# Kernel optimization log

Hardware: AMD Instinct MI355X
Metric: run time of the kernel (lower is better)

Reference implementation:

```python
import jax, jax.numpy as jnp
import numpy as np

N, L, K, Dc, Db, Dd, C = 4096, 32, 8, 64, 64, 16, 8
B, M = 32, 1000  # M_samples hardcoded to 1000 in the original forward
LOG2PI = float(np.log(2.0 * np.pi))


def setup_inputs() -> dict:
    key = jax.random.key(0)
    ks = jax.random.split(key, 16)
    X_c = jax.random.normal(ks[0], (B, Dc), dtype=jnp.float32)
    X_b = (jax.random.uniform(ks[1], (B, Db)) < 0.5).astype(jnp.float32)
    X_d = jax.random.randint(ks[2], (B, Dd), 0, C, dtype=jnp.int32)
    # variational / posterior parameters (as in __init__)
    q_z_mean = jax.random.uniform(ks[3], (N, L), dtype=jnp.float32)
    q_log_var = jax.random.uniform(ks[4], (N, L), dtype=jnp.float32)
    g = jax.random.uniform(ks[5], (N, K), dtype=jnp.float32) + 1e-3
    q_s_param = g / jnp.sum(g, axis=-1, keepdims=True)  # Dirichlet-like rows
    posterior_mean = jnp.zeros((N, L), dtype=jnp.float32)
    posterior_var = jnp.ones((N, L), dtype=jnp.float32)
    posterior_mu = jnp.ones((N, K), dtype=jnp.float32) / K
    # heterogeneous FA likelihood params (per component k)
    s = 1.0 / np.sqrt(L)
    W_g = jax.random.normal(ks[6], (K, Dc, L), dtype=jnp.float32) * s
    b_g = jax.random.normal(ks[7], (K, Dc), dtype=jnp.float32) * 0.1
    logvar_g = jax.random.normal(ks[8], (K, Dc), dtype=jnp.float32) * 0.1
    W_b = jax.random.normal(ks[9], (K, Db, L), dtype=jnp.float32) * s
    b_b = jax.random.normal(ks[10], (K, Db), dtype=jnp.float32) * 0.1
    W_d = jax.random.normal(ks[11], (K, Dd, C, L), dtype=jnp.float32) * s
    b_d = jax.random.normal(ks[12], (K, Dd, C), dtype=jnp.float32) * 0.1
    eps = jax.random.normal(ks[13], (B, M, L), dtype=jnp.float32)  # rsample noise
    return dict(index=0, X_c=X_c, X_b=X_b, X_d=X_d,
                q_z_mean=q_z_mean, q_log_var=q_log_var, q_s_param=q_s_param,
                posterior_mean=posterior_mean, posterior_var=posterior_var,
                posterior_mu=posterior_mu,
                W_g=W_g, b_g=b_g, logvar_g=logvar_g,
                W_b=W_b, b_b=b_b, W_d=W_d, b_d=b_d, eps=eps)


def _log_liks(z, X_c, X_b, X_d, W_g, b_g, logvar_g, W_b, b_b, W_d, b_d):
    # z: [B,M,L] -> each term [B,K,M] (log_pdf summed over feature dims)
    mean = jnp.einsum('kdl,bml->bkmd', W_g, z) + b_g[None, :, None, :]
    var = jnp.exp(logvar_g)[None, :, None, :]
    t1 = -0.5 * jnp.sum(LOG2PI + logvar_g[None, :, None, :]
                        + (X_c[:, None, None, :] - mean) ** 2 / var, axis=-1)
    logits_b = jnp.einsum('kdl,bml->bkmd', W_b, z) + b_b[None, :, None, :]
    t2 = jnp.sum(X_b[:, None, None, :] * logits_b - jax.nn.softplus(logits_b), axis=-1)
    logits_d = jnp.einsum('kdcl,bml->bkmdc', W_d, z) + b_d[None, :, None, :, :]
    logp = jax.nn.log_softmax(logits_d, axis=-1)  # [B,K,M,Dd,C]
    idx = jnp.broadcast_to(X_d[:, None, None, :, None].astype(jnp.int32),
                           logp.shape[:-1] + (1,))
    t3 = jnp.sum(jnp.take_along_axis(logp, idx, axis=-1)[..., 0], axis=-1)
    return t1, t2, t3


def reference(index, X_c, X_b, X_d, q_z_mean, q_log_var, q_s_param,
              posterior_mean, posterior_var, posterior_mu,
              W_g, b_g, logvar_g, W_b, b_b, W_d, b_d, eps):
    start = B * index
    end = start + B
    qm = q_z_mean[start:end]        # [B,L]
    qlv = q_log_var[start:end]      # [B,L]
    qs = q_s_param[start:end]       # [B,K]
    mp = posterior_mean[start:end]
    vp = posterior_var[start:end]
    pmu = posterior_mu[start:end]
    # reparameterized MC samples z ~ q_z
    z = qm[:, None, :] + jnp.exp(0.5 * qlv)[:, None, :] * eps  # [B,M,L]
    t1, t2, t3 = _log_liks(z, X_c, X_b, X_d, W_g, b_g, logvar_g, W_b, b_b, W_d, b_d)
    # LL_i = sum_k q_s[i,k] * sum_m (t1+t2+t3)  (sum, no /M, as in original)
    LL = jnp.sum(qs * jnp.sum(t1 + t2 + t3, axis=-1))
    # KL(q_z || p_z), both diagonal MVNs
    vq = jnp.exp(qlv)
    klz = 0.5 * jnp.sum(jnp.log(vp) - qlv + (vq + (qm - mp) ** 2) / vp - 1.0, axis=-1)
    # KL(q_s || p_s), Categorical normalizes probs
    qn = qs / jnp.sum(qs, axis=-1, keepdims=True)
    pn = pmu / jnp.sum(pmu, axis=-1, keepdims=True)
    kls = jnp.sum(qn * (jnp.log(qn) - jnp.log(pn)), axis=-1)
    elbo = LL - jnp.sum(klz) - jnp.sum(kls)
    KL_z = klz[-1]   # original returns last iteration's KL
    KL_s = kls[-1]
    term_1 = jnp.sum(t1, axis=(0, 1))  # [M]
    term_2 = jnp.sum(t2, axis=(0, 1))
    term_3 = jnp.sum(t3, axis=(0, 1))
    rik = jnp.zeros((N, K), dtype=jnp.float32).at[start:end].set(
        jax.nn.softmax(qs, axis=-1))
    rik = jax.lax.stop_gradient(rik)
    return (-elbo, LL, KL_z, KL_s, rik, term_1, term_2, term_3)
```

## Files before the change

### kernel.cpp

```cpp
#include <hip/hip_runtime.h>
#include <math.h>

#define N_ 4096
#define L_ 32
#define K_ 8
#define Dc_ 64
#define Db_ 64
#define Dd_ 16
#define C_ 8
#define B_ 32
#define M_ 1000
#define LOG2PI_ 1.8378770664093453f

#define OUT_RIK 4
#define OUT_T1 (4 + N_ * K_)

#define WS_PART 0
#define WS_LLP  98304
#define WS_WP   99328
#define WS_BIAS (WS_WP + 32768)
#define WS_IV   (WS_BIAS + 2048)
#define WS_C1   (WS_IV + 512)

typedef __attribute__((ext_vector_type(8))) short short8v;
typedef __attribute__((ext_vector_type(4))) float f32x4;

__device__ inline unsigned short f2bf(float f) {
    unsigned u = __builtin_bit_cast(unsigned, f);
    unsigned r = u + 0x7FFFu + ((u >> 16) & 1u);
    return (unsigned short)(r >> 16);
}

#define PW  65536
#define PB  (PW + 2048)
#define PIV (PB + 512)
#define PC1 (PIV + 9)

__global__ __launch_bounds__(256) void mm_prep(
    const float* __restrict__ Wg, const float* __restrict__ bg, const float* __restrict__ lvg,
    const float* __restrict__ Wb, const float* __restrict__ bb,
    const float* __restrict__ Wd, const float* __restrict__ bd,
    float* __restrict__ ws)
{
    const int t = blockIdx.x * 256 + threadIdx.x;
    unsigned short* wpw = (unsigned short*)(ws + WS_WP);

    if (t < PW) {
        int j = t & 7, lane = (t >> 3) & 63, ft = (t >> 9) & 15, k = t >> 13;
        int f = ft * 16 + (lane & 15);
        int l = (lane >> 4) * 8 + j;
        float w;
        if (f < 64)       w = Wg[((size_t)k * 64 + f) * L_ + l];
        else if (f < 128) w = Wb[((size_t)k * 64 + (f - 64)) * L_ + l];
        else { int d = (f - 128) >> 3, c = f & 7; w = Wd[(((size_t)k * 16 + d) * 8 + c) * L_ + l]; }
        wpw[t] = f2bf(w);
    } else if (t < PB) {
        int i = t - PW; int k = i >> 8, f = i & 255;
        float v;
        if (f < 64)       v = bg[k * 64 + f];
        else if (f < 128) v = bb[k * 64 + f - 64];
        else { int d = (f - 128) >> 3, c = f & 7; v = bd[(k * 16 + d) * 8 + c]; }
        ws[WS_BIAS + i] = v;
    } else if (t < PIV) {
        int i = t - PB;
        ws[WS_IV + i] = __expf(-lvg[i]);
    } else if (t < PC1) {
        int k = t - PIV;
        if (k < 8) {
            float s = 0.f;
            for (int d = 0; d < 64; ++d) s += LOG2PI_ + lvg[k * 64 + d];
            ws[WS_C1 + k] = s;
        } else {
            float s = 0.f;
            for (int i = 0; i < 512; ++i) s += LOG2PI_ + lvg[i];
            ws[WS_C1 + 8] = s;
        }
    }
}

__global__ __launch_bounds__(512) void mm_main(
    const int* __restrict__ pidx,
    const float* __restrict__ Xc, const float* __restrict__ Xb, const int* __restrict__ Xd,
    const float* __restrict__ qm_all, const float* __restrict__ qlv_all,
    const float* __restrict__ qs_all, const float* __restrict__ eps,
    float* __restrict__ ws)
{
    const int tid = threadIdx.x, w = tid >> 6, lane = tid & 63;
    const int mt = blockIdx.x, b = blockIdx.y;
    const int l15 = lane & 15, lg = lane >> 4;
    const int fr = 4 * lg;
    const int start = B_ * pidx[0];
    const unsigned short* wp = (const unsigned short*)(ws + WS_WP);

    __shared__ __align__(16) unsigned int zu[512];
    __shared__ __align__(16) float scin[2048];
    __shared__ __align__(16) float siv[512];
    __shared__ float sqk[8];
    __shared__ float sred[8][2][2][16];
    __shared__ float llred[8];

    if (tid < 256) {
        int m_loc = tid >> 3, l0 = (tid & 7) * 4;
        int m_glob = mt * 32 + m_loc;
        float4 e = make_float4(0.f, 0.f, 0.f, 0.f);
        if (m_glob < M_) e = *(const float4*)(eps + ((size_t)b * M_ + m_glob) * L_ + l0);
        float4 qm4 = *(const float4*)(qm_all + (size_t)(start + b) * L_ + l0);
        float4 ql4 = *(const float4*)(qlv_all + (size_t)(start + b) * L_ + l0);
        float z0 = qm4.x + __expf(0.5f * ql4.x) * e.x;
        float z1 = qm4.y + __expf(0.5f * ql4.y) * e.y;
        float z2 = qm4.z + __expf(0.5f * ql4.z) * e.z;
        float z3 = qm4.w + __expf(0.5f * ql4.w) * e.w;
        unsigned u0 = (unsigned)f2bf(z0) | ((unsigned)f2bf(z1) << 16);
        unsigned u1 = (unsigned)f2bf(z2) | ((unsigned)f2bf(z3) << 16);
        int widx = (m_loc >> 4) * 256 + ((l0 >> 3) * 16 + (m_loc & 15)) * 4 + ((l0 & 7) >> 1);
        zu[widx] = u0; zu[widx + 1] = u1;
    }
    {
        int f = (tid & 63) * 4;
        float4 bv = *(const float4*)(ws + WS_BIAS + tid * 4);
        if (f < 64) {
            float4 xc = *(const float4*)(Xc + b * 64 + f);
            bv.x -= xc.x; bv.y -= xc.y; bv.z -= xc.z; bv.w -= xc.w;
        }
        ((float4*)scin)[tid] = bv;
    }
    if (tid < 128) ((float4*)siv)[tid] = *(const float4*)(ws + WS_IV + tid * 4);
    if (tid < 8)   sqk[tid] = qs_all[(size_t)(start + b) * K_ + tid];
    __syncthreads();

    const short8v zb0 = *(const short8v*)((const unsigned short*)zu + lane * 8);
    const short8v zb1 = *(const short8v*)((const unsigned short*)zu + 512 + lane * 8);

    const float4 xf = *(const float4*)(Xb + b * 64 + (w & 3) * 16 + fr);
    const int d3 = 2 * w + (lg >> 1);
    const int xd = Xd[b * 16 + d3];
    const int cc0 = 4 * (lg & 1);
    float4 is3;
    is3.x = (cc0 + 0 == xd) ? 1.f : 0.f;  is3.y = (cc0 + 1 == xd) ? 1.f : 0.f;
    is3.z = (cc0 + 2 == xd) ? 1.f : 0.f;  is3.w = (cc0 + 3 == xd) ? 1.f : 0.f;

    float ta0 = 0.f, ta1 = 0.f, tb0 = 0.f, tb1 = 0.f, ll0 = 0.f, ll1 = 0.f;

    #pragma unroll 2
    for (int k = 0; k < K_; ++k) {
        const short8v wfA = *(const short8v*)(wp + ((size_t)(k * 16 + w))     * 512 + lane * 8);
        const short8v wfB = *(const short8v*)(wp + ((size_t)(k * 16 + 8 + w)) * 512 + lane * 8);
        const float4 cA = *(const float4*)(scin + k * 256 + w * 16 + fr);
        const float4 cB = *(const float4*)(scin + k * 256 + (8 + w) * 16 + fr);
        const float qkv = sqk[k];

        const f32x4 ciA = {cA.x, cA.y, cA.z, cA.w};
        const f32x4 ciB = {cB.x, cB.y, cB.z, cB.w};
        f32x4 d00 = __builtin_amdgcn_mfma_f32_16x16x32_bf16(wfA, zb0, ciA, 0, 0, 0);
        f32x4 d01 = __builtin_amdgcn_mfma_f32_16x16x32_bf16(wfA, zb1, ciA, 0, 0, 0);
        f32x4 d10 = __builtin_amdgcn_mfma_f32_16x16x32_bf16(wfB, zb0, ciB, 0, 0, 0);
        f32x4 d11 = __builtin_amdgcn_mfma_f32_16x16x32_bf16(wfB, zb1, ciB, 0, 0, 0);

        if (w < 4) {
            const float4 iv4 = *(const float4*)(siv + k * 64 + w * 16 + fr);
            float s0 = 0.f, s1 = 0.f;
            s0 = fmaf(d00[0] * d00[0], iv4.x, s0); s1 = fmaf(d01[0] * d01[0], iv4.x, s1);
            s0 = fmaf(d00[1] * d00[1], iv4.y, s0); s1 = fmaf(d01[1] * d01[1], iv4.y, s1);
            s0 = fmaf(d00[2] * d00[2], iv4.z, s0); s1 = fmaf(d01[2] * d01[2], iv4.z, s1);
            s0 = fmaf(d00[3] * d00[3], iv4.w, s0); s1 = fmaf(d01[3] * d01[3], iv4.w, s1);
            ta0 += s0; ta1 += s1;
            const float qm5 = -0.5f * qkv;
            ll0 = fmaf(qm5, s0, ll0); ll1 = fmaf(qm5, s1, ll1);
        } else {
            float s0 = 0.f, s1 = 0.f, lgt, sp;
            lgt = d00[0]; sp = fmaxf(lgt, 0.f) + __logf(1.f + __expf(-fabsf(lgt))); s0 += xf.x * lgt - sp;
            lgt = d00[1]; sp = fmaxf(lgt, 0.f) + __logf(1.f + __expf(-fabsf(lgt))); s0 += xf.y * lgt - sp;
            lgt = d00[2]; sp = fmaxf(lgt, 0.f) + __logf(1.f + __expf(-fabsf(lgt))); s0 += xf.z * lgt - sp;
            lgt = d00[3]; sp = fmaxf(lgt, 0.f) + __logf(1.f + __expf(-fabsf(lgt))); s0 += xf.w * lgt - sp;
            lgt = d01[0]; sp = fmaxf(lgt, 0.f) + __logf(1.f + __expf(-fabsf(lgt))); s1 += xf.x * lgt - sp;
            lgt = d01[1]; sp = fmaxf(lgt, 0.f) + __logf(1.f + __expf(-fabsf(lgt))); s1 += xf.y * lgt - sp;
            lgt = d01[2]; sp = fmaxf(lgt, 0.f) + __logf(1.f + __expf(-fabsf(lgt))); s1 += xf.z * lgt - sp;
            lgt = d01[3]; sp = fmaxf(lgt, 0.f) + __logf(1.f + __expf(-fabsf(lgt))); s1 += xf.w * lgt - sp;
            ta0 += s0; ta1 += s1;
            ll0 = fmaf(qkv, s0, ll0); ll1 = fmaf(qkv, s1, ll1);
        }

        {
            float e4 = __expf(d10[0]) + __expf(d10[1]) + __expf(d10[2]) + __expf(d10[3]);
            float se = e4 + __shfl_xor(e4, 16, 64);
            float u  = is3.x * d10[0] + is3.y * d10[1] + is3.z * d10[2] + is3.w * d10[3];
            float tm = u - 0.5f * __logf(se);
            tb0 += tm; ll0 = fmaf(qkv, tm, ll0);
        }
        {
            float e4 = __expf(d11[0]) + __expf(d11[1]) + __expf(d11[2]) + __expf(d11[3]);
            float se = e4 + __shfl_xor(e4, 16, 64);
            float u  = is3.x * d11[0] + is3.y * d11[1] + is3.z * d11[2] + is3.w * d11[3];
            float tm = u - 0.5f * __logf(se);
            tb1 += tm; ll1 = fmaf(qkv, tm, ll1);
        }
    }

    const bool ok0 = (mt * 32 + l15)      < M_;
    const bool ok1 = (mt * 32 + 16 + l15) < M_;
    if (!ok0) { ta0 = 0.f; tb0 = 0.f; ll0 = 0.f; }
    if (!ok1) { ta1 = 0.f; tb1 = 0.f; ll1 = 0.f; }

    float tar0 = ta0 + __shfl_xor(ta0, 16, 64); tar0 += __shfl_xor(tar0, 32, 64);
    float tar1 = ta1 + __shfl_xor(ta1, 16, 64); tar1 += __shfl_xor(tar1, 32, 64);
    float tbr0 = tb0 + __shfl_xor(tb0, 16, 64); tbr0 += __shfl_xor(tbr0, 32, 64);
    float tbr1 = tb1 + __shfl_xor(tb1, 16, 64); tbr1 += __shfl_xor(tbr1, 32, 64);
    float llv = ll0 + ll1;
    #pragma unroll
    for (int ofs = 1; ofs < 64; ofs <<= 1) llv += __shfl_xor(llv, ofs, 64);

    if (lane < 16) {
        sred[w][0][0][l15] = tar0; sred[w][1][0][l15] = tar1;
        sred[w][0][1][l15] = tbr0; sred[w][1][1][l15] = tbr1;
    }
    if (lane == 0) llred[w] = llv;
    __syncthreads();

    if (tid < 96) {
        int i = tid >> 5, tile = (tid >> 4) & 1, cx = tid & 15;
        int rt = mt * 2 + tile, m = rt * 16 + cx;
        float vout;
        if (i == 0) {
            float s = sred[0][tile][0][cx] + sred[1][tile][0][cx]
                    + sred[2][tile][0][cx] + sred[3][tile][0][cx];
            vout = (m < M_) ? (-0.5f * (ws[WS_C1 + 8] + s)) : 0.f;
        } else if (i == 1) {
            vout = sred[4][tile][0][cx] + sred[5][tile][0][cx]
                 + sred[6][tile][0][cx] + sred[7][tile][0][cx];
        } else {
            vout = 0.f;
            #pragma unroll
            for (int ww = 0; ww < 8; ++ww) vout += sred[ww][tile][1][cx];
        }
        ws[WS_PART + ((size_t)b * 64 + rt) * 48 + i * 16 + cx] = vout;
    }
    if (tid == 96) {
        float s = 0.f;
        #pragma unroll
        for (int ww = 0; ww < 8; ++ww) s += llred[ww];
        float cterm = 0.f;
        #pragma unroll
        for (int k = 0; k < 8; ++k) cterm = fmaf(sqk[k], ws[WS_C1 + k], cterm);
        int nv = M_ - mt * 32; nv = (nv > 32) ? 32 : (nv < 0 ? 0 : nv);
        ws[WS_LLP + b * 32 + mt] = s - 0.5f * cterm * (float)nv;
    }
}

__global__ __launch_bounds__(256) void mm_final(
    const int* __restrict__ pidx,
    const float* __restrict__ qm_all, const float* __restrict__ qlv_all,
    const float* __restrict__ qs_all,
    const float* __restrict__ pm_all, const float* __restrict__ pv_all,
    const float* __restrict__ pmu_all,
    const float* __restrict__ ws, float* __restrict__ out)
{
    const int tid = threadIdx.x;
    if (blockIdx.x == 0) {
        __shared__ float wred[4];
        __shared__ float skl[B_], sks[B_];
        const int start = B_ * pidx[0];
        float v = ws[WS_LLP + tid] + ws[WS_LLP + 256 + tid]
                + ws[WS_LLP + 512 + tid] + ws[WS_LLP + 768 + tid];
        #pragma unroll
        for (int ofs = 1; ofs < 64; ofs <<= 1) v += __shfl_xor(v, ofs, 64);
        if ((tid & 63) == 0) wred[tid >> 6] = v;

        if (tid < B_) {
            int r = start + tid;
            float kl = 0.f;
            for (int l = 0; l < L_; ++l) {
                float qmv = qm_all[(size_t)r * L_ + l];
                float qlv = qlv_all[(size_t)r * L_ + l];
                float mp  = pm_all[(size_t)r * L_ + l];
                float vp  = pv_all[(size_t)r * L_ + l];
                float d   = qmv - mp;
                kl += __logf(vp) - qlv + (__expf(qlv) + d * d) / vp - 1.f;
            }
            skl[tid] = 0.5f * kl;

            float qsum = 0.f, psum = 0.f;
            #pragma unroll
            for (int j = 0; j < K_; ++j) {
                qsum += qs_all[(size_t)r * K_ + j];
                psum += pmu_all[(size_t)r * K_ + j];
            }
            float ks = 0.f;
            #pragma unroll
            for (int j = 0; j < K_; ++j) {
                float qn = qs_all[(size_t)r * K_ + j] / qsum;
                float pn = pmu_all[(size_t)r * K_ + j] / psum;
                ks += qn * (__logf(qn) - __logf(pn));
            }
            sks[tid] = ks;
        }
        __syncthreads();
        if (tid == 0) {
            float LL = wred[0] + wred[1] + wred[2] + wred[3];
            float sklz = 0.f, skls = 0.f;
            for (int i = 0; i < B_; ++i) { sklz += skl[i]; skls += sks[i]; }
            float elbo = LL - sklz - skls;
            out[0] = -elbo;
            out[1] = LL;
            out[2] = skl[B_ - 1];
            out[3] = sks[B_ - 1];
        }
    } else if (blockIdx.x <= 12) {
        int g = (blockIdx.x - 1) * 256 + tid;
        if (g < 3 * M_) {
            int i = g / M_, m = g % M_;
            int rt = m >> 4, cx = m & 15;
            float s = 0.f;
            #pragma unroll 8
            for (int b2 = 0; b2 < 32; ++b2)
                s += ws[WS_PART + ((size_t)b2 * 64 + rt) * 48 + i * 16 + cx];
            out[OUT_T1 + i * M_ + m] = s;
        }
    } else {
        int i = (blockIdx.x - 13) * 256 + tid;
        int r = i >> 3, c = i & 7;
        int start = B_ * pidx[0];
        float v = 0.f;
        if (r >= start && r < start + B_) {
            const float* row = qs_all + (size_t)r * K_;
            float mx = row[0];
            #pragma unroll
            for (int jj = 1; jj < K_; ++jj) mx = fmaxf(mx, row[jj]);
            float se = 0.f;
            #pragma unroll
            for (int jj = 0; jj < K_; ++jj) se += __expf(row[jj] - mx);
            v = __expf(row[c] - mx) / se;
        }
        out[OUT_RIK + i] = v;
    }
}

extern "C" void kernel_launch(void* const* d_in, const int* in_sizes, int n_in,
                              void* d_out, int out_size, void* d_ws, size_t ws_size,
                              hipStream_t stream)
{
    (void)in_sizes; (void)n_in; (void)out_size; (void)ws_size;
    const int*   pidx = (const int*)d_in[0];
    const float* Xc   = (const float*)d_in[1];
    const float* Xb   = (const float*)d_in[2];
    const int*   Xd   = (const int*)d_in[3];
    const float* qm   = (const float*)d_in[4];
    const float* qlv  = (const float*)d_in[5];
    const float* qs   = (const float*)d_in[6];
    const float* pm   = (const float*)d_in[7];
    const float* pv   = (const float*)d_in[8];
    const float* pmu  = (const float*)d_in[9];
    const float* Wg   = (const float*)d_in[10];
    const float* bg   = (const float*)d_in[11];
    const float* lvg  = (const float*)d_in[12];
    const float* Wb   = (const float*)d_in[13];
    const float* bb   = (const float*)d_in[14];
    const float* Wd   = (const float*)d_in[15];
    const float* bd   = (const float*)d_in[16];
    const float* eps  = (const float*)d_in[17];
    float* out = (float*)d_out;
    float* ws  = (float*)d_ws;

    mm_prep<<<(PC1 + 255) / 256, 256, 0, stream>>>(Wg, bg, lvg, Wb, bb, Wd, bd, ws);

    dim3 grid(32, 32);
    mm_main<<<grid, 512, 0, stream>>>(pidx, Xc, Xb, Xd, qm, qlv, qs, eps, ws);

    mm_final<<<141, 256, 0, stream>>>(pidx, qm, qlv, qs, pm, pv, pmu, ws, out);
}
```

Baseline: 42.25 us.

## Fuse prep, main and final kernels into one with last-block atomic reduction

Removes the separate weight-packing prep kernel and the final reduction kernel. The main kernel now reads fp32 weights directly and converts them to bf16 in registers, computes bias and inverse-variance tables inline, and writes the rik softmax rows. The final reductions run in the last block to finish, detected with atomic counters that a memset zeroes before launch. This saves two kernel launches and the intermediate workspace round trip. In exchange every block repeats the weight loads and conversions, and the reduction tail is serialized on the last-arriving blocks.

```diff
diff --git a/kernel.cpp b/kernel.cpp
--- a/kernel.cpp
+++ b/kernel.cpp
@@ -1,4 +1,5 @@
 #include <hip/hip_runtime.h>
+#include <hip/hip_bf16.h>
 #include <math.h>
 
 #define N_ 4096
@@ -17,10 +18,7 @@
 
 #define WS_PART 0
 #define WS_LLP  98304
-#define WS_WP   99328
-#define WS_BIAS (WS_WP + 32768)
-#define WS_IV   (WS_BIAS + 2048)
-#define WS_C1   (WS_IV + 512)
+#define WS_CNT  99328
 
 typedef __attribute__((ext_vector_type(8))) short short8v;
 typedef __attribute__((ext_vector_type(4))) float f32x4;
@@ -31,66 +29,39 @@
     return (unsigned short)(r >> 16);
 }
 
-#define PW  65536
-#define PB  (PW + 2048)
-#define PIV (PB + 512)
-#define PC1 (PIV + 9)
-
-__global__ __launch_bounds__(256) void mm_prep(
+__device__ inline unsigned short bf16u(float x) {
+    __hip_bfloat16 h = __float2bfloat16(x);
+    return __builtin_bit_cast(unsigned short, h);
+}
+
+__device__ inline short8v cvt8(float4 a, float4 b) {
+    short8v r;
+    r[0] = (short)bf16u(a.x); r[1] = (short)bf16u(a.y);
+    r[2] = (short)bf16u(a.z); r[3] = (short)bf16u(a.w);
+    r[4] = (short)bf16u(b.x); r[5] = (short)bf16u(b.y);
+    r[6] = (short)bf16u(b.z); r[7] = (short)bf16u(b.w);
+    return r;
+}
+
+__global__ __launch_bounds__(512) void mm_fused(
+    const int* __restrict__ pidx,
+    const float* __restrict__ Xc, const float* __restrict__ Xb, const int* __restrict__ Xd,
+    const float* __restrict__ qm_all, const float* __restrict__ qlv_all,
+    const float* __restrict__ qs_all,
+    const float* __restrict__ pm_all, const float* __restrict__ pv_all,
+    const float* __restrict__ pmu_all,
     const float* __restrict__ Wg, const float* __restrict__ bg, const float* __restrict__ lvg,
     const float* __restrict__ Wb, const float* __restrict__ bb,
     const float* __restrict__ Wd, const float* __restrict__ bd,
-    float* __restrict__ ws)
-{
-    const int t = blockIdx.x * 256 + threadIdx.x;
-    unsigned short* wpw = (unsigned short*)(ws + WS_WP);
-
-    if (t < PW) {
-        int j = t & 7, lane = (t >> 3) & 63, ft = (t >> 9) & 15, k = t >> 13;
-        int f = ft * 16 + (lane & 15);
-        int l = (lane >> 4) * 8 + j;
-        float w;
-        if (f < 64)       w = Wg[((size_t)k * 64 + f) * L_ + l];
-        else if (f < 128) w = Wb[((size_t)k * 64 + (f - 64)) * L_ + l];
-        else { int d = (f - 128) >> 3, c = f & 7; w = Wd[(((size_t)k * 16 + d) * 8 + c) * L_ + l]; }
-        wpw[t] = f2bf(w);
-    } else if (t < PB) {
-        int i = t - PW; int k = i >> 8, f = i & 255;
-        float v;
-        if (f < 64)       v = bg[k * 64 + f];
-        else if (f < 128) v = bb[k * 64 + f - 64];
-        else { int d = (f - 128) >> 3, c = f & 7; v = bd[(k * 16 + d) * 8 + c]; }
-        ws[WS_BIAS + i] = v;
-    } else if (t < PIV) {
-        int i = t - PB;
-        ws[WS_IV + i] = __expf(-lvg[i]);
-    } else if (t < PC1) {
-        int k = t - PIV;
-        if (k < 8) {
-            float s = 0.f;
-            for (int d = 0; d < 64; ++d) s += LOG2PI_ + lvg[k * 64 + d];
-            ws[WS_C1 + k] = s;
-        } else {
-            float s = 0.f;
-            for (int i = 0; i < 512; ++i) s += LOG2PI_ + lvg[i];
-            ws[WS_C1 + 8] = s;
-        }
-    }
-}
-
-__global__ __launch_bounds__(512) void mm_main(
-    const int* __restrict__ pidx,
-    const float* __restrict__ Xc, const float* __restrict__ Xb, const int* __restrict__ Xd,
-    const float* __restrict__ qm_all, const float* __restrict__ qlv_all,
-    const float* __restrict__ qs_all, const float* __restrict__ eps,
-    float* __restrict__ ws)
+    const float* __restrict__ eps,
+    float* __restrict__ out, float* __restrict__ ws)
 {
     const int tid = threadIdx.x, w = tid >> 6, lane = tid & 63;
     const int mt = blockIdx.x, b = blockIdx.y;
     const int l15 = lane & 15, lg = lane >> 4;
     const int fr = 4 * lg;
     const int start = B_ * pidx[0];
-    const unsigned short* wp = (const unsigned short*)(ws + WS_WP);
+    unsigned* cnt = (unsigned*)(ws + WS_CNT);
 
     __shared__ __align__(16) unsigned int zu[512];
     __shared__ __align__(16) float scin[2048];
@@ -98,6 +69,9 @@
     __shared__ float sqk[8];
     __shared__ float sred[8][2][2][16];
     __shared__ float llred[8];
+    __shared__ int sflag;
+    __shared__ float sfin[8], sll[8], sc1k[8], sllc[4];
+    __shared__ float skl2[B_], sks2[B_];
 
     if (tid < 256) {
         int m_loc = tid >> 3, l0 = (tid & 7) * 4;
@@ -116,16 +90,27 @@
         zu[widx] = u0; zu[widx + 1] = u1;
     }
     {
-        int f = (tid & 63) * 4;
-        float4 bv = *(const float4*)(ws + WS_BIAS + tid * 4);
+        int k = tid >> 6, f = (tid & 63) * 4;
+        float4 bv;
         if (f < 64) {
+            bv = *(const float4*)(bg + k * 64 + f);
             float4 xc = *(const float4*)(Xc + b * 64 + f);
             bv.x -= xc.x; bv.y -= xc.y; bv.z -= xc.z; bv.w -= xc.w;
+        } else if (f < 128) {
+            bv = *(const float4*)(bb + k * 64 + (f - 64));
+        } else {
+            bv = *(const float4*)(bd + k * 128 + (f - 128));
         }
         ((float4*)scin)[tid] = bv;
     }
-    if (tid < 128) ((float4*)siv)[tid] = *(const float4*)(ws + WS_IV + tid * 4);
-    if (tid < 8)   sqk[tid] = qs_all[(size_t)(start + b) * K_ + tid];
+    if (tid < 128) {
+        float4 lv4 = *(const float4*)(lvg + tid * 4);
+        float4 r;
+        r.x = __expf(-lv4.x); r.y = __expf(-lv4.y);
+        r.z = __expf(-lv4.z); r.w = __expf(-lv4.w);
+        ((float4*)siv)[tid] = r;
+    }
+    if (tid < 8) sqk[tid] = qs_all[(size_t)(start + b) * K_ + tid];
     __syncthreads();
 
     const short8v zb0 = *(const short8v*)((const unsigned short*)zu + lane * 8);
@@ -139,12 +124,20 @@
     is3.x = (cc0 + 0 == xd) ? 1.f : 0.f;  is3.y = (cc0 + 1 == xd) ? 1.f : 0.f;
     is3.z = (cc0 + 2 == xd) ? 1.f : 0.f;  is3.w = (cc0 + 3 == xd) ? 1.f : 0.f;
 
+    const float* baseA = (w < 4) ? Wg : Wb;
+    const size_t offA = (size_t)((w & 3) * 16 + l15) * 32 + lg * 8;
+    const size_t offB = (size_t)(w * 16 + l15) * 32 + lg * 8;
+
     float ta0 = 0.f, ta1 = 0.f, tb0 = 0.f, tb1 = 0.f, ll0 = 0.f, ll1 = 0.f;
 
     #pragma unroll 2
     for (int k = 0; k < K_; ++k) {
-        const short8v wfA = *(const short8v*)(wp + ((size_t)(k * 16 + w))     * 512 + lane * 8);
-        const short8v wfB = *(const short8v*)(wp + ((size_t)(k * 16 + 8 + w)) * 512 + lane * 8);
+        float4 ra0 = *(const float4*)(baseA + k * 2048 + offA);
+        float4 ra1 = *(const float4*)(baseA + k * 2048 + offA + 4);
+        float4 rb0 = *(const float4*)(Wd + k * 4096 + offB);
+        float4 rb1 = *(const float4*)(Wd + k * 4096 + offB + 4);
+        const short8v wfA = cvt8(ra0, ra1);
+        const short8v wfB = cvt8(rb0, rb1);
         const float4 cA = *(const float4*)(scin + k * 256 + w * 16 + fr);
         const float4 cB = *(const float4*)(scin + k * 256 + (8 + w) * 16 + fr);
         const float qkv = sqk[k];
@@ -218,12 +211,11 @@
 
     if (tid < 96) {
         int i = tid >> 5, tile = (tid >> 4) & 1, cx = tid & 15;
-        int rt = mt * 2 + tile, m = rt * 16 + cx;
+        int rt = mt * 2 + tile;
         float vout;
         if (i == 0) {
-            float s = sred[0][tile][0][cx] + sred[1][tile][0][cx]
-                    + sred[2][tile][0][cx] + sred[3][tile][0][cx];
-            vout = (m < M_) ? (-0.5f * (ws[WS_C1 + 8] + s)) : 0.f;
+            vout = sred[0][tile][0][cx] + sred[1][tile][0][cx]
+                 + sred[2][tile][0][cx] + sred[3][tile][0][cx];
         } else if (i == 1) {
             vout = sred[4][tile][0][cx] + sred[5][tile][0][cx]
                  + sred[6][tile][0][cx] + sred[7][tile][0][cx];
@@ -238,33 +230,78 @@
         float s = 0.f;
         #pragma unroll
         for (int ww = 0; ww < 8; ++ww) s += llred[ww];
-        float cterm = 0.f;
-        #pragma unroll
-        for (int k = 0; k < 8; ++k) cterm = fmaf(sqk[k], ws[WS_C1 + k], cterm);
-        int nv = M_ - mt * 32; nv = (nv > 32) ? 32 : (nv < 0 ? 0 : nv);
-        ws[WS_LLP + b * 32 + mt] = s - 0.5f * cterm * (float)nv;
-    }
-}
-
-__global__ __launch_bounds__(256) void mm_final(
-    const int* __restrict__ pidx,
-    const float* __restrict__ qm_all, const float* __restrict__ qlv_all,
-    const float* __restrict__ qs_all,
-    const float* __restrict__ pm_all, const float* __restrict__ pv_all,
-    const float* __restrict__ pmu_all,
-    const float* __restrict__ ws, float* __restrict__ out)
-{
-    const int tid = threadIdx.x;
-    if (blockIdx.x == 0) {
-        __shared__ float wred[4];
-        __shared__ float skl[B_], sks[B_];
-        const int start = B_ * pidx[0];
-        float v = ws[WS_LLP + tid] + ws[WS_LLP + 256 + tid]
-                + ws[WS_LLP + 512 + tid] + ws[WS_LLP + 768 + tid];
+        ws[WS_LLP + b * 32 + mt] = s;
+    }
+
+    if (tid < 32) {
+        int i = (b * 32 + mt) * 32 + tid;
+        int r = i >> 3, c = i & 7;
+        float v = 0.f;
+        if (r >= start && r < start + B_) {
+            const float* row = qs_all + (size_t)r * K_;
+            float mx = row[0];
+            #pragma unroll
+            for (int jj = 1; jj < K_; ++jj) mx = fmaxf(mx, row[jj]);
+            float se = 0.f;
+            #pragma unroll
+            for (int jj = 0; jj < K_; ++jj) se += __expf(row[jj] - mx);
+            v = __expf(row[c] - mx) / se;
+        }
+        out[OUT_RIK + i] = v;
+    }
+
+    __syncthreads();
+    if (tid == 0) {
+        __threadfence();
+        unsigned o1 = atomicAdd(cnt + mt, 1u);
+        unsigned o2 = atomicAdd(cnt + 32, 1u);
+        sflag = ((o1 == 31u) ? 1 : 0) | ((o2 == 1023u) ? 2 : 0);
+    }
+    __syncthreads();
+    const int flg = sflag;
+
+    if (flg & 1) {
+        __threadfence();
+        float c1v = LOG2PI_ + lvg[tid];
+        #pragma unroll
+        for (int ofs = 1; ofs < 64; ofs <<= 1) c1v += __shfl_xor(c1v, ofs, 64);
+        if (lane == 0) sfin[w] = c1v;
+        __syncthreads();
+        float C1sum = 0.f;
+        #pragma unroll
+        for (int ww = 0; ww < 8; ++ww) C1sum += sfin[ww];
+        if (tid < 96) {
+            int i = tid >> 5, cx = tid & 31;
+            int m = mt * 32 + cx;
+            if (m < M_) {
+                int rt = mt * 2 + (cx >> 4), cxx = cx & 15;
+                float s = 0.f;
+                #pragma unroll 8
+                for (int b2 = 0; b2 < 32; ++b2)
+                    s += ws[WS_PART + ((size_t)b2 * 64 + rt) * 48 + i * 16 + cxx];
+                float vout = (i == 0) ? (-0.5f * (32.f * C1sum + s)) : s;
+                out[OUT_T1 + i * M_ + m] = vout;
+            }
+        }
+    }
+
+    if (flg & 2) {
+        __threadfence();
+        float v = ws[WS_LLP + tid] + ws[WS_LLP + 512 + tid];
         #pragma unroll
         for (int ofs = 1; ofs < 64; ofs <<= 1) v += __shfl_xor(v, ofs, 64);
-        if ((tid & 63) == 0) wred[tid >> 6] = v;
-
+        if (lane == 0) sll[w] = v;
+        float c1v = LOG2PI_ + lvg[tid];
+        #pragma unroll
+        for (int ofs = 1; ofs < 64; ofs <<= 1) c1v += __shfl_xor(c1v, ofs, 64);
+        if (lane == 0) sc1k[w] = c1v;
+        __syncthreads();
+        if (tid < 256) {
+            float lc = qs_all[(size_t)(start + (tid >> 3)) * K_ + (tid & 7)] * sc1k[tid & 7];
+            #pragma unroll
+            for (int ofs = 1; ofs < 64; ofs <<= 1) lc += __shfl_xor(lc, ofs, 64);
+            if (lane == 0) sllc[w] = lc;
+        }
         if (tid < B_) {
             int r = start + tid;
             float kl = 0.f;
@@ -276,8 +313,7 @@
                 float d   = qmv - mp;
                 kl += __logf(vp) - qlv + (__expf(qlv) + d * d) / vp - 1.f;
             }
-            skl[tid] = 0.5f * kl;
-
+            skl2[tid] = 0.5f * kl;
             float qsum = 0.f, psum = 0.f;
             #pragma unroll
             for (int j = 0; j < K_; ++j) {
@@ -291,46 +327,25 @@
                 float pn = pmu_all[(size_t)r * K_ + j] / psum;
                 ks += qn * (__logf(qn) - __logf(pn));
             }
-            sks[tid] = ks;
+            sks2[tid] = ks;
         }
         __syncthreads();
         if (tid == 0) {
-            float LL = wred[0] + wred[1] + wred[2] + wred[3];
+            float LL = 0.f;
+            #pragma unroll
+            for (int ww = 0; ww < 8; ++ww) LL += sll[ww];
+            float lcs = 0.f;
+            #pragma unroll
+            for (int ww = 0; ww < 4; ++ww) lcs += sllc[ww];
+            LL -= 0.5f * (float)M_ * lcs;
             float sklz = 0.f, skls = 0.f;
-            for (int i = 0; i < B_; ++i) { sklz += skl[i]; skls += sks[i]; }
+            for (int i = 0; i < B_; ++i) { sklz += skl2[i]; skls += sks2[i]; }
             float elbo = LL - sklz - skls;
             out[0] = -elbo;
             out[1] = LL;
-            out[2] = skl[B_ - 1];
-            out[3] = sks[B_ - 1];
-        }
-    } else if (blockIdx.x <= 12) {
-        int g = (blockIdx.x - 1) * 256 + tid;
-        if (g < 3 * M_) {
-            int i = g / M_, m = g % M_;
-            int rt = m >> 4, cx = m & 15;
-            float s = 0.f;
-            #pragma unroll 8
-            for (int b2 = 0; b2 < 32; ++b2)
-                s += ws[WS_PART + ((size_t)b2 * 64 + rt) * 48 + i * 16 + cx];
-            out[OUT_T1 + i * M_ + m] = s;
-        }
-    } else {
-        int i = (blockIdx.x - 13) * 256 + tid;
-        int r = i >> 3, c = i & 7;
-        int start = B_ * pidx[0];
-        float v = 0.f;
-        if (r >= start && r < start + B_) {
-            const float* row = qs_all + (size_t)r * K_;
-            float mx = row[0];
-            #pragma unroll
-            for (int jj = 1; jj < K_; ++jj) mx = fmaxf(mx, row[jj]);
-            float se = 0.f;
-            #pragma unroll
-            for (int jj = 0; jj < K_; ++jj) se += __expf(row[jj] - mx);
-            v = __expf(row[c] - mx) / se;
-        }
-        out[OUT_RIK + i] = v;
+            out[2] = skl2[B_ - 1];
+            out[3] = sks2[B_ - 1];
+        }
     }
 }
 
@@ -360,10 +375,10 @@
     float* out = (float*)d_out;
     float* ws  = (float*)d_ws;
 
-    mm_prep<<<(PC1 + 255) / 256, 256, 0, stream>>>(Wg, bg, lvg, Wb, bb, Wd, bd, ws);
+    hipMemsetAsync((char*)d_ws + (size_t)WS_CNT * 4, 0, 33 * 4, stream);
 
     dim3 grid(32, 32);
-    mm_main<<<grid, 512, 0, stream>>>(pidx, Xc, Xb, Xd, qm, qlv, qs, eps, ws);
-
-    mm_final<<<141, 256, 0, stream>>>(pidx, qm, qlv, qs, pm, pv, pmu, ws, out);
-}
+    mm_fused<<<grid, 512, 0, stream>>>(pidx, Xc, Xb, Xd, qm, qlv, qs,
+                                       pm, pv, pmu, Wg, bg, lvg, Wb, bb, Wd, bd,
+                                       eps, out, ws);
+}
```

New measurement: 79.23 us. 1.88x slower.

## Process 64 samples per block to reuse weight fragments across four MFMA tiles

Applied to the files above, without the earlier changes.

Each mm_main block now covers 64 Monte Carlo samples instead of 32. Every loaded weight fragment and bias feeds four MFMAs instead of two, and the grid shrinks to 16x32 blocks, with launch_bounds set to request two blocks per CU. The Gaussian constant offset moves from mm_main into mm_final's reduction, scaled by the batch size. The intent is to halve weight loads and block setup, at the cost of more registers per thread and fewer blocks (512) to spread over the CUs.

```diff
diff --git a/kernel.cpp b/kernel.cpp
--- a/kernel.cpp
+++ b/kernel.cpp
@@ -78,7 +78,7 @@
     }
 }
 
-__global__ __launch_bounds__(512) void mm_main(
+__global__ __launch_bounds__(512, 2) void mm_main(
     const int* __restrict__ pidx,
     const float* __restrict__ Xc, const float* __restrict__ Xb, const int* __restrict__ Xd,
     const float* __restrict__ qm_all, const float* __restrict__ qlv_all,
@@ -92,16 +92,16 @@
     const int start = B_ * pidx[0];
     const unsigned short* wp = (const unsigned short*)(ws + WS_WP);
 
-    __shared__ __align__(16) unsigned int zu[512];
+    __shared__ __align__(16) unsigned int zu[1024];
     __shared__ __align__(16) float scin[2048];
     __shared__ __align__(16) float siv[512];
     __shared__ float sqk[8];
-    __shared__ float sred[8][2][2][16];
+    __shared__ float sred[8][4][2][16];
     __shared__ float llred[8];
 
-    if (tid < 256) {
+    {
         int m_loc = tid >> 3, l0 = (tid & 7) * 4;
-        int m_glob = mt * 32 + m_loc;
+        int m_glob = mt * 64 + m_loc;
         float4 e = make_float4(0.f, 0.f, 0.f, 0.f);
         if (m_glob < M_) e = *(const float4*)(eps + ((size_t)b * M_ + m_glob) * L_ + l0);
         float4 qm4 = *(const float4*)(qm_all + (size_t)(start + b) * L_ + l0);
@@ -128,8 +128,11 @@
     if (tid < 8)   sqk[tid] = qs_all[(size_t)(start + b) * K_ + tid];
     __syncthreads();
 
-    const short8v zb0 = *(const short8v*)((const unsigned short*)zu + lane * 8);
-    const short8v zb1 = *(const short8v*)((const unsigned short*)zu + 512 + lane * 8);
+    const unsigned short* zp = (const unsigned short*)zu;
+    const short8v zbA = *(const short8v*)(zp + lane * 8);
+    const short8v zbB = *(const short8v*)(zp + 512 + lane * 8);
+    const short8v zbC = *(const short8v*)(zp + 1024 + lane * 8);
+    const short8v zbD = *(const short8v*)(zp + 1536 + lane * 8);
 
     const float4 xf = *(const float4*)(Xb + b * 64 + (w & 3) * 16 + fr);
     const int d3 = 2 * w + (lg >> 1);
@@ -139,7 +142,32 @@
     is3.x = (cc0 + 0 == xd) ? 1.f : 0.f;  is3.y = (cc0 + 1 == xd) ? 1.f : 0.f;
     is3.z = (cc0 + 2 == xd) ? 1.f : 0.f;  is3.w = (cc0 + 3 == xd) ? 1.f : 0.f;
 
-    float ta0 = 0.f, ta1 = 0.f, tb0 = 0.f, tb1 = 0.f, ll0 = 0.f, ll1 = 0.f;
+    float taA = 0.f, taB = 0.f, taC = 0.f, taD = 0.f;
+    float tbA = 0.f, tbB = 0.f, tbC = 0.f, tbD = 0.f;
+    float llA = 0.f, llB = 0.f, llC = 0.f, llD = 0.f;
+
+#define GAUSS_EPI(dd, ta_, ll_) { \
+    float s_ = 0.f; \
+    s_ = fmaf(dd[0] * dd[0], iv4.x, s_); \
+    s_ = fmaf(dd[1] * dd[1], iv4.y, s_); \
+    s_ = fmaf(dd[2] * dd[2], iv4.z, s_); \
+    s_ = fmaf(dd[3] * dd[3], iv4.w, s_); \
+    ta_ += s_; ll_ = fmaf(qm5, s_, ll_); }
+
+#define BERN_EPI(dd, ta_, ll_) { \
+    float s_ = 0.f, lgt_, sp_; \
+    lgt_ = dd[0]; sp_ = fmaxf(lgt_, 0.f) + __logf(1.f + __expf(-fabsf(lgt_))); s_ += xf.x * lgt_ - sp_; \
+    lgt_ = dd[1]; sp_ = fmaxf(lgt_, 0.f) + __logf(1.f + __expf(-fabsf(lgt_))); s_ += xf.y * lgt_ - sp_; \
+    lgt_ = dd[2]; sp_ = fmaxf(lgt_, 0.f) + __logf(1.f + __expf(-fabsf(lgt_))); s_ += xf.z * lgt_ - sp_; \
+    lgt_ = dd[3]; sp_ = fmaxf(lgt_, 0.f) + __logf(1.f + __expf(-fabsf(lgt_))); s_ += xf.w * lgt_ - sp_; \
+    ta_ += s_; ll_ = fmaf(qkv, s_, ll_); }
+
+#define CAT_EPI(dd, tb_, ll_) { \
+    float e4_ = __expf(dd[0]) + __expf(dd[1]) + __expf(dd[2]) + __expf(dd[3]); \
+    float se_ = e4_ + __shfl_xor(e4_, 16, 64); \
+    float u_  = is3.x * dd[0] + is3.y * dd[1] + is3.z * dd[2] + is3.w * dd[3]; \
+    float tm_ = u_ - 0.5f * __logf(se_); \
+    tb_ += tm_; ll_ = fmaf(qkv, tm_, ll_); }
 
     #pragma unroll 2
     for (int k = 0; k < K_; ++k) {
@@ -151,98 +179,87 @@
 
         const f32x4 ciA = {cA.x, cA.y, cA.z, cA.w};
         const f32x4 ciB = {cB.x, cB.y, cB.z, cB.w};
-        f32x4 d00 = __builtin_amdgcn_mfma_f32_16x16x32_bf16(wfA, zb0, ciA, 0, 0, 0);
-        f32x4 d01 = __builtin_amdgcn_mfma_f32_16x16x32_bf16(wfA, zb1, ciA, 0, 0, 0);
-        f32x4 d10 = __builtin_amdgcn_mfma_f32_16x16x32_bf16(wfB, zb0, ciB, 0, 0, 0);
-        f32x4 d11 = __builtin_amdgcn_mfma_f32_16x16x32_bf16(wfB, zb1, ciB, 0, 0, 0);
+        f32x4 dA0 = __builtin_amdgcn_mfma_f32_16x16x32_bf16(wfA, zbA, ciA, 0, 0, 0);
+        f32x4 dA1 = __builtin_amdgcn_mfma_f32_16x16x32_bf16(wfA, zbB, ciA, 0, 0, 0);
+        f32x4 dA2 = __builtin_amdgcn_mfma_f32_16x16x32_bf16(wfA, zbC, ciA, 0, 0, 0);
+        f32x4 dA3 = __builtin_amdgcn_mfma_f32_16x16x32_bf16(wfA, zbD, ciA, 0, 0, 0);
+        f32x4 dB0 = __builtin_amdgcn_mfma_f32_16x16x32_bf16(wfB, zbA, ciB, 0, 0, 0);
+        f32x4 dB1 = __builtin_amdgcn_mfma_f32_16x16x32_bf16(wfB, zbB, ciB, 0, 0, 0);
+        f32x4 dB2 = __builtin_amdgcn_mfma_f32_16x16x32_bf16(wfB, zbC, ciB, 0, 0, 0);
+        f32x4 dB3 = __builtin_amdgcn_mfma_f32_16x16x32_bf16(wfB, zbD, ciB, 0, 0, 0);
 
         if (w < 4) {
             const float4 iv4 = *(const float4*)(siv + k * 64 + w * 16 + fr);
-            float s0 = 0.f, s1 = 0.f;
-            s0 = fmaf(d00[0] * d00[0], iv4.x, s0); s1 = fmaf(d01[0] * d01[0], iv4.x, s1);
-            s0 = fmaf(d00[1] * d00[1], iv4.y, s0); s1 = fmaf(d01[1] * d01[1], iv4.y, s1);
-            s0 = fmaf(d00[2] * d00[2], iv4.z, s0); s1 = fmaf(d01[2] * d01[2], iv4.z, s1);
-            s0 = fmaf(d00[3] * d00[3], iv4.w, s0); s1 = fmaf(d01[3] * d01[3], iv4.w, s1);
-            ta0 += s0; ta1 += s1;
             const float qm5 = -0.5f * qkv;
-            ll0 = fmaf(qm5, s0, ll0); ll1 = fmaf(qm5, s1, ll1);
+            GAUSS_EPI(dA0, taA, llA)
+            GAUSS_EPI(dA1, taB, llB)
+            GAUSS_EPI(dA2, taC, llC)
+            GAUSS_EPI(dA3, taD, llD)
         } else {
-            float s0 = 0.f, s1 = 0.f, lgt, sp;
-            lgt = d00[0]; sp = fmaxf(lgt, 0.f) + __logf(1.f + __expf(-fabsf(lgt))); s0 += xf.x * lgt - sp;
-            lgt = d00[1]; sp = fmaxf(lgt, 0.f) + __logf(1.f + __expf(-fabsf(lgt))); s0 += xf.y * lgt - sp;
-            lgt = d00[2]; sp = fmaxf(lgt, 0.f) + __logf(1.f + __expf(-fabsf(lgt))); s0 += xf.z * lgt - sp;
-            lgt = d00[3]; sp = fmaxf(lgt, 0.f) + __logf(1.f + __expf(-fabsf(lgt))); s0 += xf.w * lgt - sp;
-            lgt = d01[0]; sp = fmaxf(lgt, 0.f) + __logf(1.f + __expf(-fabsf(lgt))); s1 += xf.x * lgt - sp;
-            lgt = d01[1]; sp = fmaxf(lgt, 0.f) + __logf(1.f + __expf(-fabsf(lgt))); s1 += xf.y * lgt - sp;
-            lgt = d01[2]; sp = fmaxf(lgt, 0.f) + __logf(1.f + __expf(-fabsf(lgt))); s1 += xf.z * lgt - sp;
-            lgt = d01[3]; sp = fmaxf(lgt, 0.f) + __logf(1.f + __expf(-fabsf(lgt))); s1 += xf.w * lgt - sp;
-            ta0 += s0; ta1 += s1;
-            ll0 = fmaf(qkv, s0, ll0); ll1 = fmaf(qkv, s1, ll1);
-        }
-
-        {
-            float e4 = __expf(d10[0]) + __expf(d10[1]) + __expf(d10[2]) + __expf(d10[3]);
-            float se = e4 + __shfl_xor(e4, 16, 64);
-            float u  = is3.x * d10[0] + is3.y * d10[1] + is3.z * d10[2] + is3.w * d10[3];
-            float tm = u - 0.5f * __logf(se);
-            tb0 += tm; ll0 = fmaf(qkv, tm, ll0);
-        }
-        {
-            float e4 = __expf(d11[0]) + __expf(d11[1]) + __expf(d11[2]) + __expf(d11[3]);
-            float se = e4 + __shfl_xor(e4, 16, 64);
-            float u  = is3.x * d11[0] + is3.y * d11[1] + is3.z * d11[2] + is3.w * d11[3];
-            float tm = u - 0.5f * __logf(se);
-            tb1 += tm; ll1 = fmaf(qkv, tm, ll1);
-        }
-    }
-
-    const bool ok0 = (mt * 32 + l15)      < M_;
-    const bool ok1 = (mt * 32 + 16 + l15) < M_;
-    if (!ok0) { ta0 = 0.f; tb0 = 0.f; ll0 = 0.f; }
-    if (!ok1) { ta1 = 0.f; tb1 = 0.f; ll1 = 0.f; }
-
-    float tar0 = ta0 + __shfl_xor(ta0, 16, 64); tar0 += __shfl_xor(tar0, 32, 64);
-    float tar1 = ta1 + __shfl_xor(ta1, 16, 64); tar1 += __shfl_xor(tar1, 32, 64);
-    float tbr0 = tb0 + __shfl_xor(tb0, 16, 64); tbr0 += __shfl_xor(tbr0, 32, 64);
-    float tbr1 = tb1 + __shfl_xor(tb1, 16, 64); tbr1 += __shfl_xor(tbr1, 32, 64);
-    float llv = ll0 + ll1;
+            BERN_EPI(dA0, taA, llA)
+            BERN_EPI(dA1, taB, llB)
+            BERN_EPI(dA2, taC, llC)
+            BERN_EPI(dA3, taD, llD)
+        }
+        CAT_EPI(dB0, tbA, llA)
+        CAT_EPI(dB1, tbB, llB)
+        CAT_EPI(dB2, tbC, llC)
+        CAT_EPI(dB3, tbD, llD)
+    }
+
+    const int mrow = mt * 64 + l15;
+    if (mrow      >= M_) { taA = 0.f; tbA = 0.f; llA = 0.f; }
+    if (mrow + 16 >= M_) { taB = 0.f; tbB = 0.f; llB = 0.f; }
+    if (mrow + 32 >= M_) { taC = 0.f; tbC = 0.f; llC = 0.f; }
+    if (mrow + 48 >= M_) { taD = 0.f; tbD = 0.f; llD = 0.f; }
+
+    float tarA = taA + __shfl_xor(taA, 16, 64); tarA += __shfl_xor(tarA, 32, 64);
+    float tarB = taB + __shfl_xor(taB, 16, 64); tarB += __shfl_xor(tarB, 32, 64);
+    float tarC = taC + __shfl_xor(taC, 16, 64); tarC += __shfl_xor(tarC, 32, 64);
+    float tarD = taD + __shfl_xor(taD, 16, 64); tarD += __shfl_xor(tarD, 32, 64);
+    float tbrA = tbA + __shfl_xor(tbA, 16, 64); tbrA += __shfl_xor(tbrA, 32, 64);
+    float tbrB = tbB + __shfl_xor(tbB, 16, 64); tbrB += __shfl_xor(tbrB, 32, 64);
+    float tbrC = tbC + __shfl_xor(tbC, 16, 64); tbrC += __shfl_xor(tbrC, 32, 64);
+    float tbrD = tbD + __shfl_xor(tbD, 16, 64); tbrD += __shfl_xor(tbrD, 32, 64);
+    float llv = llA + llB + llC + llD;
     #pragma unroll
     for (int ofs = 1; ofs < 64; ofs <<= 1) llv += __shfl_xor(llv, ofs, 64);
 
     if (lane < 16) {
-        sred[w][0][0][l15] = tar0; sred[w][1][0][l15] = tar1;
-        sred[w][0][1][l15] = tbr0; sred[w][1][1][l15] = tbr1;
+        sred[w][0][0][l15] = tarA; sred[w][1][0][l15] = tarB;
+        sred[w][2][0][l15] = tarC; sred[w][3][0][l15] = tarD;
+        sred[w][0][1][l15] = tbrA; sred[w][1][1][l15] = tbrB;
+        sred[w][2][1][l15] = tbrC; sred[w][3][1][l15] = tbrD;
     }
     if (lane == 0) llred[w] = llv;
     __syncthreads();
 
-    if (tid < 96) {
-        int i = tid >> 5, tile = (tid >> 4) & 1, cx = tid & 15;
-        int rt = mt * 2 + tile, m = rt * 16 + cx;
-        float vout;
+    if (tid < 192) {
+        int i = tid >> 6, tile = (tid >> 4) & 3, cx = tid & 15;
+        int rt = mt * 4 + tile;
+        float s;
         if (i == 0) {
-            float s = sred[0][tile][0][cx] + sred[1][tile][0][cx]
-                    + sred[2][tile][0][cx] + sred[3][tile][0][cx];
-            vout = (m < M_) ? (-0.5f * (ws[WS_C1 + 8] + s)) : 0.f;
+            s = sred[0][tile][0][cx] + sred[1][tile][0][cx]
+              + sred[2][tile][0][cx] + sred[3][tile][0][cx];
         } else if (i == 1) {
-            vout = sred[4][tile][0][cx] + sred[5][tile][0][cx]
-                 + sred[6][tile][0][cx] + sred[7][tile][0][cx];
+            s = sred[4][tile][0][cx] + sred[5][tile][0][cx]
+              + sred[6][tile][0][cx] + sred[7][tile][0][cx];
         } else {
-            vout = 0.f;
-            #pragma unroll
-            for (int ww = 0; ww < 8; ++ww) vout += sred[ww][tile][1][cx];
-        }
-        ws[WS_PART + ((size_t)b * 64 + rt) * 48 + i * 16 + cx] = vout;
-    }
-    if (tid == 96) {
+            s = 0.f;
+            #pragma unroll
+            for (int ww = 0; ww < 8; ++ww) s += sred[ww][tile][1][cx];
+        }
+        ws[WS_PART + ((size_t)b * 64 + rt) * 48 + i * 16 + cx] = s;
+    }
+    if (tid == 192) {
         float s = 0.f;
         #pragma unroll
         for (int ww = 0; ww < 8; ++ww) s += llred[ww];
         float cterm = 0.f;
         #pragma unroll
         for (int k = 0; k < 8; ++k) cterm = fmaf(sqk[k], ws[WS_C1 + k], cterm);
-        int nv = M_ - mt * 32; nv = (nv > 32) ? 32 : (nv < 0 ? 0 : nv);
-        ws[WS_LLP + b * 32 + mt] = s - 0.5f * cterm * (float)nv;
+        int nv = M_ - mt * 64; nv = (nv > 64) ? 64 : (nv < 0 ? 0 : nv);
+        ws[WS_LLP + b * 16 + mt] = s - 0.5f * cterm * (float)nv;
     }
 }
 
@@ -259,8 +276,7 @@
         __shared__ float wred[4];
         __shared__ float skl[B_], sks[B_];
         const int start = B_ * pidx[0];
-        float v = ws[WS_LLP + tid] + ws[WS_LLP + 256 + tid]
-                + ws[WS_LLP + 512 + tid] + ws[WS_LLP + 768 + tid];
+        float v = ws[WS_LLP + tid] + ws[WS_LLP + 256 + tid];
         #pragma unroll
         for (int ofs = 1; ofs < 64; ofs <<= 1) v += __shfl_xor(v, ofs, 64);
         if ((tid & 63) == 0) wred[tid >> 6] = v;
@@ -313,6 +329,7 @@
             #pragma unroll 8
             for (int b2 = 0; b2 < 32; ++b2)
                 s += ws[WS_PART + ((size_t)b2 * 64 + rt) * 48 + i * 16 + cx];
+            if (i == 0) s = -0.5f * (32.f * ws[WS_C1 + 8] + s);
             out[OUT_T1 + i * M_ + m] = s;
         }
     } else {
@@ -362,7 +379,7 @@
 
     mm_prep<<<(PC1 + 255) / 256, 256, 0, stream>>>(Wg, bg, lvg, Wb, bb, Wd, bd, ws);
 
-    dim3 grid(32, 32);
+    dim3 grid(16, 32);
     mm_main<<<grid, 512, 0, stream>>>(pidx, Xc, Xb, Xd, qm, qlv, qs, eps, ws);
 
     mm_final<<<141, 256, 0, stream>>>(pidx, qm, qlv, qs, pm, pv, pmu, ws, out);
```

Measured after the change: 41.57 us. About the same (-1.6%).
